# Performance work log

Measured on AMD Instinct MI355X. Metric: run time of the kernel, lower is better.

The kernel has to match this reference:

```python
import jax, jax.numpy as jnp
import numpy as np

NUM_LEVELS = 16
RESOLUTIONS = np.array([16, 18, 20, 22, 25, 27, 30, 34, 38, 42, 47, 52, 58, 64, 72, 80], dtype=np.int32)
OFFSETS = np.concatenate([np.zeros(1, np.int64), np.cumsum(RESOLUTIONS.astype(np.int64) ** 3)]).astype(np.int32)
BATCH = 2
C_IN = 16
C_OUT = 16
K = 3


def setup_inputs() -> dict:
    key = jax.random.key(0)
    k1, k2, k3 = jax.random.split(key, 3)
    n_total = int(OFFSETS[-1])  # 1846083 embeddings across all levels
    inp = jax.random.normal(k1, (BATCH, n_total, C_IN), dtype=jnp.float32)
    weight = 0.1 * jax.random.normal(k2, (NUM_LEVELS, K, K, K, C_IN, C_OUT), dtype=jnp.float32)
    bias = 0.01 * jax.random.uniform(k3, (NUM_LEVELS, C_OUT), dtype=jnp.float32)
    # offsets / resolutions are static int buffers (kept as numpy so they stay
    # concrete under jit, mirroring registered int buffers in the torch module)
    return {"input": inp, "weight": weight, "bias": bias,
            "offsets": OFFSETS, "resolutions": RESOLUTIONS}


def _conv_all_levels(inp, weight, bias, offsets, resolutions):
    # inp: [B, N_total, C_in]; per level l the slice offsets[l]:offsets[l+1]
    # is a dense R_l^3 grid flattened x-fastest (idx = x + y*R + z*R^2).
    B = inp.shape[0]
    dn = ('NDHWC', 'DHWIO', 'NDHWC')
    outs = []
    for l in range(NUM_LEVELS):
        R = int(resolutions[l])
        off = int(offsets[l])
        x = inp[:, off:off + R ** 3, :].reshape(B, R, R, R, C_IN)  # [B,Z,Y,X,Cin]
        y = jax.lax.conv_general_dilated(
            x, weight[l], window_strides=(1, 1, 1), padding='SAME',
            dimension_numbers=dn)  # zero-padded 3x3x3 neighborhood gather
        y = y + bias[l]
        outs.append(y.reshape(B, R ** 3, C_OUT))
    return jnp.concatenate(outs, axis=1)  # [B, N_total, C_out]


def reference(input, weight, bias, offsets, resolutions):
    return _conv_all_levels(input, weight, bias, offsets, resolutions)
```

## Files before the change

### kernel.cpp

```cpp
#include <hip/hip_runtime.h>

#define NLVL 16
#define NTOT 1846083
#define NBLK 4376

typedef float  f32x4  __attribute__((ext_vector_type(4)));
typedef __bf16 bf16x8 __attribute__((ext_vector_type(8)));
typedef __bf16 bf16x4 __attribute__((ext_vector_type(4)));
typedef unsigned int u32x4 __attribute__((ext_vector_type(4)));

__constant__ int c_R[NLVL]   = {16,18,20,22,25,27,30,34,38,42,47,52,58,64,72,80};
__constant__ int c_off[NLVL] = {0,4096,9928,17928,28576,44201,63884,90884,130188,185060,259148,362971,503579,698691,960835,1334083};
__constant__ int c_czy[NLVL] = {4,5,5,6,7,7,8,9,10,11,12,13,15,16,18,20};
__constant__ int c_cx[NLVL]  = {1,2,2,2,2,2,2,3,3,3,3,4,4,4,5,5};
__constant__ int c_base[17]  = {0,1000,1900,2412,2892,3308,3524,3722,3902,4064,4128,4184,4240,4288,4328,4368,4376};

__device__ __align__(16) unsigned short g_bfrag[NLVL*3*5*64*8];

__global__ void prep_bfrag(const float* __restrict__ wgt) {
    int tid = blockIdx.x * 256 + threadIdx.x;
    if (tid >= NLVL*3*5*64) return;
    int lane = tid & 63;
    int p    = (tid >> 6) % 5;
    int d    = (tid / (5*64)) % 3;
    int l    = tid / (3*5*64);
    int quad = lane >> 4, co = lane & 15;
    unsigned short v[8];
#pragma unroll
    for (int j = 0; j < 8; ++j) {
        int k   = quad*8 + j;
        int tip = k >> 4;
        int ci  = k & 15;
        int t2  = 2*p + tip;
        float f = (t2 < 9) ? wgt[((l*27 + d*9 + t2)*16 + ci)*16 + co] : 0.f;
        v[j] = __builtin_bit_cast(unsigned short, (__bf16)f);
    }
    u32x4 pk;
    pk[0] = (unsigned)v[0] | ((unsigned)v[1] << 16);
    pk[1] = (unsigned)v[2] | ((unsigned)v[3] << 16);
    pk[2] = (unsigned)v[4] | ((unsigned)v[5] << 16);
    pk[3] = (unsigned)v[6] | ((unsigned)v[7] << 16);
    *(u32x4*)&g_bfrag[(size_t)tid*8] = pk;
}

__global__ __launch_bounds__(256, 3)
void conv_kernel(const float* __restrict__ in,
                 const float* __restrict__ bias,
                 float* __restrict__ out) {
    __shared__ __align__(16) __bf16 slab[2*1728];

    const int bid = blockIdx.x;
    int idx = 0;
#pragma unroll
    for (int i = 1; i < 16; ++i) if (bid >= c_base[i]) idx = i;
    const int l = 15 - idx;
    const int R = c_R[l], off = c_off[l], czy = c_czy[l], cx = c_cx[l];

    int local = bid - c_base[idx];
    int per_b = czy*cx*cx;
    int bb = local / per_b;         int r1 = local - bb*per_b;
    int zt = r1 / (czy*cx);         int r2 = r1 - zt*(czy*cx);
    int yt = r2 / cx;               int xt = r2 - yt*cx;
    const int z0 = zt*16;
    const int z1 = (z0 + 16 < R) ? z0 + 16 : R;
    const int y0 = yt*4, x0 = xt*16;

    const int t    = threadIdx.x;
    const int lane = t & 63;
    const int wv   = t >> 6;
    const int quad = lane >> 4;
    const int co   = lane & 15;
    const int m    = lane & 15;
    const int qh   = quad >> 1;

    bf16x8 bfr[15];
#pragma unroll
    for (int d = 0; d < 3; ++d)
#pragma unroll
        for (int p = 0; p < 5; ++p)
            bfr[d*5+p] = *(const bf16x8*)&g_bfrag[(size_t)(((l*3 + d)*5 + p)*64 + lane)*8];

    const int albase = wv*576 + m*32 + (quad & 1)*16;
    int aoff[5];
    {
        const int T0[5] = {0, 64, 608, 1152, 1216};
        const int T1[5] = {32, 576, 640, 1184, 1216};
#pragma unroll
        for (int p = 0; p < 5; ++p) aoff[p] = albase + (qh ? T1[p] : T0[p]);
    }

    const long zs = (long)R*R*16;
    long g0 = 0, g1 = 0; int lo0 = 0, lo1 = 0; bool yx0 = false, yx1 = false;
    {
        int c = t;
        int yp = c/72; int rem = c - yp*72; int xp = rem>>2; int ci4 = (rem&3)<<2;
        lo0 = (yp*18 + xp)*16 + ci4;
        int y = y0 + yp - 1, x = x0 + xp - 1;
        yx0 = ((unsigned)y < (unsigned)R) && ((unsigned)x < (unsigned)R);
        g0 = ((long)bb*NTOT + off)*16 + ((long)y*R + x)*16 + ci4;
    }
    const bool has1 = (t < 176);
    if (has1) {
        int c = t + 256;
        int yp = c/72; int rem = c - yp*72; int xp = rem>>2; int ci4 = (rem&3)<<2;
        lo1 = (yp*18 + xp)*16 + ci4;
        int y = y0 + yp - 1, x = x0 + xp - 1;
        yx1 = ((unsigned)y < (unsigned)R) && ((unsigned)x < (unsigned)R);
        g1 = ((long)bb*NTOT + off)*16 + ((long)y*R + x)*16 + ci4;
    }

    __bf16* sbr = slab;
    __bf16* sbw = slab + 1728;

    {
        int zn = z0 - 1;
        bool zok = (unsigned)zn < (unsigned)R;
        f32x4 v0 = {0,0,0,0}, v1 = {0,0,0,0};
        if (zok && yx0) v0 = *(const f32x4*)(in + g0 + (long)zn*zs);
        if (has1 && zok && yx1) v1 = *(const f32x4*)(in + g1 + (long)zn*zs);
        bf16x4 h0 = {(__bf16)v0[0],(__bf16)v0[1],(__bf16)v0[2],(__bf16)v0[3]};
        *(bf16x4*)(sbr + lo0) = h0;
        if (has1) {
            bf16x4 h1 = {(__bf16)v1[0],(__bf16)v1[1],(__bf16)v1[2],(__bf16)v1[3]};
            *(bf16x4*)(sbr + lo1) = h1;
        }
    }
    __syncthreads();

    const bool ywok = (y0 + wv) < R;
    const float bv = bias[(l << 4) + co];
    const long obase = ((long)bb*NTOT + off)*16;

    f32x4 accA = {0,0,0,0}, accB = {0,0,0,0}, accC = {0,0,0,0};
    const int steps = z1 - z0 + 2;

    for (int i = 0; i < steps; ++i) {
        const int zp = z0 - 1 + i;
        const int zn = zp + 1;
        const bool sok = (zn <= z1);

        f32x4 v0 = {0,0,0,0}, v1 = {0,0,0,0};
        if (sok) {
            bool zok = (unsigned)zn < (unsigned)R;
            if (zok && yx0) v0 = *(const f32x4*)(in + g0 + (long)zn*zs);
            if (has1 && zok && yx1) v1 = *(const f32x4*)(in + g1 + (long)zn*zs);
        }

        const char* sb = (const char*)sbr;
#pragma unroll
        for (int p = 0; p < 5; ++p) {
            bf16x8 a = *(const bf16x8*)(sb + aoff[p]);
            accC = __builtin_amdgcn_mfma_f32_16x16x32_bf16(a, bfr[p],      accC, 0, 0, 0);
            accB = __builtin_amdgcn_mfma_f32_16x16x32_bf16(a, bfr[5+p],  accB, 0, 0, 0);
            accA = __builtin_amdgcn_mfma_f32_16x16x32_bf16(a, bfr[10+p], accA, 0, 0, 0);
        }

        if (sok) {
            bf16x4 h0 = {(__bf16)v0[0],(__bf16)v0[1],(__bf16)v0[2],(__bf16)v0[3]};
            *(bf16x4*)(sbw + lo0) = h0;
            if (has1) {
                bf16x4 h1 = {(__bf16)v1[0],(__bf16)v1[1],(__bf16)v1[2],(__bf16)v1[3]};
                *(bf16x4*)(sbw + lo1) = h1;
            }
        }

        if (i >= 2 && ywok) {
            int z = zp - 1;
            long rb = obase + (((long)z*R + (y0 + wv))*R)*16 + co;
#pragma unroll
            for (int rr = 0; rr < 4; ++rr) {
                int x = x0 + quad*4 + rr;
                if (x < R) out[rb + (long)x*16] = accA[rr] + bv;
            }
        }

        accA = accB; accB = accC;
        accC = (f32x4){0,0,0,0};

        __syncthreads();
        __bf16* tmp = sbr; sbr = sbw; sbw = tmp;
    }
}

extern "C" void kernel_launch(void* const* d_in, const int* in_sizes, int n_in,
                              void* d_out, int out_size, void* d_ws, size_t ws_size,
                              hipStream_t stream) {
    const float* inp = (const float*)d_in[0];
    const float* wgt = (const float*)d_in[1];
    const float* bia = (const float*)d_in[2];
    float* out = (float*)d_out;
    prep_bfrag<<<dim3((NLVL*3*5*64 + 255)/256), dim3(256), 0, stream>>>(wgt);
    conv_kernel<<<dim3(NBLK), dim3(256), 0, stream>>>(inp, bia, out);
}
```

Measured before the change: 439.6 us.

## Prefetch input slices two planes ahead and vectorize output stores via swapped MFMA

Restructures the z-plane loop so global loads for plane z+2 are issued while plane z+1 is converted and written to shared memory, using two register sets rotated by a 2-way unrolled loop. This hides global load latency behind the MFMA work. It also swaps the MFMA operand order so each lane holds four consecutive output channels, which allows one 16-byte store per lane with a vector bias add instead of four scalar strided stores. The full __syncthreads is replaced with an LDS-only waitcnt plus a raw barrier, so in-flight global loads are not drained at each step. The cost is extra registers.

```diff
diff --git a/kernel.cpp b/kernel.cpp
--- a/kernel.cpp
+++ b/kernel.cpp
@@ -69,7 +69,6 @@
     const int lane = t & 63;
     const int wv   = t >> 6;
     const int quad = lane >> 4;
-    const int co   = lane & 15;
     const int m    = lane & 15;
     const int qh   = quad >> 1;
 
@@ -112,74 +111,81 @@
     __bf16* sbr = slab;
     __bf16* sbw = slab + 1728;
 
+    const f32x4 zero4 = {0,0,0,0};
+    f32x4 rA0 = zero4, rA1 = zero4, rB0 = zero4, rB1 = zero4;
+
     {
         int zn = z0 - 1;
-        bool zok = (unsigned)zn < (unsigned)R;
-        f32x4 v0 = {0,0,0,0}, v1 = {0,0,0,0};
-        if (zok && yx0) v0 = *(const f32x4*)(in + g0 + (long)zn*zs);
-        if (has1 && zok && yx1) v1 = *(const f32x4*)(in + g1 + (long)zn*zs);
-        bf16x4 h0 = {(__bf16)v0[0],(__bf16)v0[1],(__bf16)v0[2],(__bf16)v0[3]};
+        if (zn >= 0) {
+            if (yx0) rA0 = *(const f32x4*)(in + g0 + (long)zn*zs);
+            if (has1 && yx1) rA1 = *(const f32x4*)(in + g1 + (long)zn*zs);
+        }
+        if (yx0) rB0 = *(const f32x4*)(in + g0 + (long)z0*zs);
+        if (has1 && yx1) rB1 = *(const f32x4*)(in + g1 + (long)z0*zs);
+        bf16x4 h0 = {(__bf16)rA0[0],(__bf16)rA0[1],(__bf16)rA0[2],(__bf16)rA0[3]};
         *(bf16x4*)(sbr + lo0) = h0;
         if (has1) {
-            bf16x4 h1 = {(__bf16)v1[0],(__bf16)v1[1],(__bf16)v1[2],(__bf16)v1[3]};
+            bf16x4 h1 = {(__bf16)rA1[0],(__bf16)rA1[1],(__bf16)rA1[2],(__bf16)rA1[3]};
             *(bf16x4*)(sbr + lo1) = h1;
         }
     }
-    __syncthreads();
+    asm volatile("s_waitcnt lgkmcnt(0)" ::: "memory");
+    __builtin_amdgcn_s_barrier();
+    asm volatile("" ::: "memory");
 
     const bool ywok = (y0 + wv) < R;
-    const float bv = bias[(l << 4) + co];
+    const f32x4 bv4 = *(const f32x4*)(bias + (l << 4) + (quad << 2));
     const long obase = ((long)bb*NTOT + off)*16;
-
-    f32x4 accA = {0,0,0,0}, accB = {0,0,0,0}, accC = {0,0,0,0};
     const int steps = z1 - z0 + 2;
 
-    for (int i = 0; i < steps; ++i) {
-        const int zp = z0 - 1 + i;
-        const int zn = zp + 1;
-        const bool sok = (zn <= z1);
-
-        f32x4 v0 = {0,0,0,0}, v1 = {0,0,0,0};
-        if (sok) {
-            bool zok = (unsigned)zn < (unsigned)R;
-            if (zok && yx0) v0 = *(const f32x4*)(in + g0 + (long)zn*zs);
-            if (has1 && zok && yx1) v1 = *(const f32x4*)(in + g1 + (long)zn*zs);
-        }
-
+    f32x4 accA = zero4, accB = zero4, accC = zero4;
+
+    auto stepf = [&](int i, f32x4& w0, f32x4& w1, f32x4& l0, f32x4& l1) {
+        const int zl = z0 + 1 + i;
+        if (zl <= z1) {
+            const bool zok = zl < R;
+            l0 = zero4; l1 = zero4;
+            if (zok && yx0) l0 = *(const f32x4*)(in + g0 + (long)zl*zs);
+            if (has1 && zok && yx1) l1 = *(const f32x4*)(in + g1 + (long)zl*zs);
+        }
+        if (i <= steps - 2) {
+            bf16x4 h0 = {(__bf16)w0[0],(__bf16)w0[1],(__bf16)w0[2],(__bf16)w0[3]};
+            *(bf16x4*)(sbw + lo0) = h0;
+            if (has1) {
+                bf16x4 h1 = {(__bf16)w1[0],(__bf16)w1[1],(__bf16)w1[2],(__bf16)w1[3]};
+                *(bf16x4*)(sbw + lo1) = h1;
+            }
+        }
         const char* sb = (const char*)sbr;
 #pragma unroll
         for (int p = 0; p < 5; ++p) {
             bf16x8 a = *(const bf16x8*)(sb + aoff[p]);
-            accC = __builtin_amdgcn_mfma_f32_16x16x32_bf16(a, bfr[p],      accC, 0, 0, 0);
-            accB = __builtin_amdgcn_mfma_f32_16x16x32_bf16(a, bfr[5+p],  accB, 0, 0, 0);
-            accA = __builtin_amdgcn_mfma_f32_16x16x32_bf16(a, bfr[10+p], accA, 0, 0, 0);
-        }
-
-        if (sok) {
-            bf16x4 h0 = {(__bf16)v0[0],(__bf16)v0[1],(__bf16)v0[2],(__bf16)v0[3]};
-            *(bf16x4*)(sbw + lo0) = h0;
-            if (has1) {
-                bf16x4 h1 = {(__bf16)v1[0],(__bf16)v1[1],(__bf16)v1[2],(__bf16)v1[3]};
-                *(bf16x4*)(sbw + lo1) = h1;
+            accC = __builtin_amdgcn_mfma_f32_16x16x32_bf16(bfr[p],    a, accC, 0, 0, 0);
+            accB = __builtin_amdgcn_mfma_f32_16x16x32_bf16(bfr[5+p],  a, accB, 0, 0, 0);
+            accA = __builtin_amdgcn_mfma_f32_16x16x32_bf16(bfr[10+p], a, accA, 0, 0, 0);
+        }
+        if (i >= 2 && ywok) {
+            const int x = x0 + m;
+            if (x < R) {
+                const int z = z0 - 2 + i;
+                long rb = obase + (((long)z*R + (y0 + wv))*(long)R + x)*16 + (quad << 2);
+                f32x4 o = accA + bv4;
+                *(f32x4*)(out + rb) = o;
             }
         }
-
-        if (i >= 2 && ywok) {
-            int z = zp - 1;
-            long rb = obase + (((long)z*R + (y0 + wv))*R)*16 + co;
-#pragma unroll
-            for (int rr = 0; rr < 4; ++rr) {
-                int x = x0 + quad*4 + rr;
-                if (x < R) out[rb + (long)x*16] = accA[rr] + bv;
-            }
-        }
-
-        accA = accB; accB = accC;
-        accC = (f32x4){0,0,0,0};
-
-        __syncthreads();
-        __bf16* tmp = sbr; sbr = sbw; sbw = tmp;
-    }
+        accA = accB; accB = accC; accC = zero4;
+        asm volatile("s_waitcnt lgkmcnt(0)" ::: "memory");
+        __builtin_amdgcn_s_barrier();
+        asm volatile("" ::: "memory");
+        __bf16* t_ = sbr; sbr = sbw; sbw = t_;
+    };
+
+    int i = 0;
+    for (; i + 1 < steps; i += 2) {
+        stepf(i,     rB0, rB1, rA0, rA1);
+        stepf(i + 1, rA0, rA1, rB0, rB1);
+    }
+    if (i < steps) stepf(i, rB0, rB1, rA0, rA1);
 }
 
 extern "C" void kernel_launch(void* const* d_in, const int* in_sizes, int n_in,
```

After: 429.4 us. 2.3% less time.

## Stream fp32 input slabs into LDS via async global_load_lds with triple buffering

Applied to the files above, without the earlier changes.

Replaces the register-staged load plus bf16 conversion into a double-buffered bf16 slab with direct async global-to-LDS loads into a triple-buffered fp32 slab, converting to bf16 when reading A fragments. Tiles grow to 8 y-rows per block (two rows per wave), halving the block count and reusing the weight fragments across two MFMA chains. MFMA operands are swapped so the output is stored as 16-byte vectors, and the barrier waits on vmcnt to keep one slab in flight. This costs more LDS per block (fp32 instead of bf16, three buffers) and adds conversion work on every LDS read, while raising launch bounds to 4 waves per SIMD.

```diff
diff --git a/kernel.cpp b/kernel.cpp
--- a/kernel.cpp
+++ b/kernel.cpp
@@ -2,20 +2,21 @@
 
 #define NLVL 16
 #define NTOT 1846083
-#define NBLK 4376
+#define NBLK 2254
 
 typedef float  f32x4  __attribute__((ext_vector_type(4)));
 typedef __bf16 bf16x8 __attribute__((ext_vector_type(8)));
-typedef __bf16 bf16x4 __attribute__((ext_vector_type(4)));
+typedef unsigned int u32;
 typedef unsigned int u32x4 __attribute__((ext_vector_type(4)));
 
 __constant__ int c_R[NLVL]   = {16,18,20,22,25,27,30,34,38,42,47,52,58,64,72,80};
 __constant__ int c_off[NLVL] = {0,4096,9928,17928,28576,44201,63884,90884,130188,185060,259148,362971,503579,698691,960835,1334083};
-__constant__ int c_czy[NLVL] = {4,5,5,6,7,7,8,9,10,11,12,13,15,16,18,20};
+__constant__ int c_czy[NLVL] = {2,3,3,3,4,4,4,5,5,6,6,7,8,8,9,10};
 __constant__ int c_cx[NLVL]  = {1,2,2,2,2,2,2,3,3,3,3,4,4,4,5,5};
-__constant__ int c_base[17]  = {0,1000,1900,2412,2892,3308,3524,3722,3902,4064,4128,4184,4240,4288,4328,4368,4376};
+__constant__ int c_base[17]  = {0,500,950,1206,1462,1686,1794,1902,1992,2082,2114,2146,2178,2202,2226,2250,2254};
 
 __device__ __align__(16) unsigned short g_bfrag[NLVL*3*5*64*8];
+__device__ __align__(16) float g_zero[4] = {0.f, 0.f, 0.f, 0.f};
 
 __global__ void prep_bfrag(const float* __restrict__ wgt) {
     int tid = blockIdx.x * 256 + threadIdx.x;
@@ -36,18 +37,24 @@
         v[j] = __builtin_bit_cast(unsigned short, (__bf16)f);
     }
     u32x4 pk;
-    pk[0] = (unsigned)v[0] | ((unsigned)v[1] << 16);
-    pk[1] = (unsigned)v[2] | ((unsigned)v[3] << 16);
-    pk[2] = (unsigned)v[4] | ((unsigned)v[5] << 16);
-    pk[3] = (unsigned)v[6] | ((unsigned)v[7] << 16);
+    pk[0] = (u32)v[0] | ((u32)v[1] << 16);
+    pk[1] = (u32)v[2] | ((u32)v[3] << 16);
+    pk[2] = (u32)v[4] | ((u32)v[5] << 16);
+    pk[3] = (u32)v[6] | ((u32)v[7] << 16);
     *(u32x4*)&g_bfrag[(size_t)tid*8] = pk;
 }
 
-__global__ __launch_bounds__(256, 3)
+__device__ __forceinline__ void gll16(const void* g, void* l) {
+    __builtin_amdgcn_global_load_lds(
+        (const __attribute__((address_space(1))) u32*)g,
+        (__attribute__((address_space(3))) u32*)l, 16, 0, 0);
+}
+
+__global__ __launch_bounds__(256, 4)
 void conv_kernel(const float* __restrict__ in,
                  const float* __restrict__ bias,
                  float* __restrict__ out) {
-    __shared__ __align__(16) __bf16 slab[2*1728];
+    __shared__ __align__(16) float slab[3*2880];
 
     const int bid = blockIdx.x;
     int idx = 0;
@@ -63,13 +70,12 @@
     int yt = r2 / cx;               int xt = r2 - yt*cx;
     const int z0 = zt*16;
     const int z1 = (z0 + 16 < R) ? z0 + 16 : R;
-    const int y0 = yt*4, x0 = xt*16;
+    const int y0 = yt*8, x0 = xt*16;
 
     const int t    = threadIdx.x;
     const int lane = t & 63;
     const int wv   = t >> 6;
     const int quad = lane >> 4;
-    const int co   = lane & 15;
     const int m    = lane & 15;
     const int qh   = quad >> 1;
 
@@ -80,106 +86,116 @@
         for (int p = 0; p < 5; ++p)
             bfr[d*5+p] = *(const bf16x8*)&g_bfrag[(size_t)(((l*3 + d)*5 + p)*64 + lane)*8];
 
-    const int albase = wv*576 + m*32 + (quad & 1)*16;
+    const int albase = wv*2304 + m*64 + (quad & 1)*32;
     int aoff[5];
     {
-        const int T0[5] = {0, 64, 608, 1152, 1216};
-        const int T1[5] = {32, 576, 640, 1184, 1216};
+        const int T0[5] = {0, 128, 1216, 2304, 2432};
+        const int T1[5] = {64, 1152, 1280, 2368, 2432};
 #pragma unroll
         for (int p = 0; p < 5; ++p) aoff[p] = albase + (qh ? T1[p] : T0[p]);
     }
 
     const long zs = (long)R*R*16;
-    long g0 = 0, g1 = 0; int lo0 = 0, lo1 = 0; bool yx0 = false, yx1 = false;
+    const long gstart = ((long)bb*NTOT + off)*16;
+    const float* cur[3]; bool ok[3];
     {
-        int c = t;
-        int yp = c/72; int rem = c - yp*72; int xp = rem>>2; int ci4 = (rem&3)<<2;
-        lo0 = (yp*18 + xp)*16 + ci4;
-        int y = y0 + yp - 1, x = x0 + xp - 1;
-        yx0 = ((unsigned)y < (unsigned)R) && ((unsigned)x < (unsigned)R);
-        g0 = ((long)bb*NTOT + off)*16 + ((long)y*R + x)*16 + ci4;
-    }
-    const bool has1 = (t < 176);
-    if (has1) {
-        int c = t + 256;
-        int yp = c/72; int rem = c - yp*72; int xp = rem>>2; int ci4 = (rem&3)<<2;
-        lo1 = (yp*18 + xp)*16 + ci4;
-        int y = y0 + yp - 1, x = x0 + xp - 1;
-        yx1 = ((unsigned)y < (unsigned)R) && ((unsigned)x < (unsigned)R);
-        g1 = ((long)bb*NTOT + off)*16 + ((long)y*R + x)*16 + ci4;
-    }
-
-    __bf16* sbr = slab;
-    __bf16* sbw = slab + 1728;
+#pragma unroll
+        for (int s = 0; s < 3; ++s) {
+            int c = t + s*256;
+            int yp = c/72; int rem = c - yp*72; int xp = rem>>2; int ci4 = (rem&3)<<2;
+            int y = y0 + yp - 1, x = x0 + xp - 1;
+            ok[s] = ((unsigned)y < (unsigned)R) && ((unsigned)x < (unsigned)R);
+            cur[s] = in + gstart + ((long)y*R + x)*16 + ci4 + (long)(z0-1)*zs;
+        }
+    }
+    const bool has2 = (t < 208);
+
+    float* b0 = slab;
+    float* b1 = slab + 2880;
+    float* b2 = slab + 5760;
+
+    const float* zv = g_zero;
+    char* const lw = (char*)0 + wv*1024;
+    const int wvo = wv*1024;
 
     {
-        int zn = z0 - 1;
-        bool zok = (unsigned)zn < (unsigned)R;
-        f32x4 v0 = {0,0,0,0}, v1 = {0,0,0,0};
-        if (zok && yx0) v0 = *(const f32x4*)(in + g0 + (long)zn*zs);
-        if (has1 && zok && yx1) v1 = *(const f32x4*)(in + g1 + (long)zn*zs);
-        bf16x4 h0 = {(__bf16)v0[0],(__bf16)v0[1],(__bf16)v0[2],(__bf16)v0[3]};
-        *(bf16x4*)(sbr + lo0) = h0;
-        if (has1) {
-            bf16x4 h1 = {(__bf16)v1[0],(__bf16)v1[1],(__bf16)v1[2],(__bf16)v1[3]};
-            *(bf16x4*)(sbr + lo1) = h1;
-        }
-    }
-    __syncthreads();
-
-    const bool ywok = (y0 + wv) < R;
-    const float bv = bias[(l << 4) + co];
-    const long obase = ((long)bb*NTOT + off)*16;
-
-    f32x4 accA = {0,0,0,0}, accB = {0,0,0,0}, accC = {0,0,0,0};
+        bool zrA = (z0 - 1) >= 0;
+        gll16(zrA && ok[0] ? cur[0] : zv, (char*)b0 + wvo);
+        gll16(zrA && ok[1] ? cur[1] : zv, (char*)b0 + wvo + 4096);
+        if (has2) gll16(zrA && ok[2] ? cur[2] : zv, (char*)b0 + wvo + 8192);
+        gll16(ok[0] ? cur[0] + zs : zv, (char*)b1 + wvo);
+        gll16(ok[1] ? cur[1] + zs : zv, (char*)b1 + wvo + 4096);
+        if (has2) gll16(ok[2] ? cur[2] + zs : zv, (char*)b1 + wvo + 8192);
+        cur[0] += 2*zs; cur[1] += 2*zs; cur[2] += 2*zs;
+    }
+    asm volatile("s_waitcnt vmcnt(3)" ::: "memory");
+    __builtin_amdgcn_s_barrier();
+    asm volatile("" ::: "memory");
+
+    const int yo0 = y0 + 2*wv, yo1 = yo0 + 1;
+    const bool yw0 = yo0 < R, yw1 = yo1 < R;
+    const bool xok = (x0 + m) < R;
+    const f32x4 bv4 = *(const f32x4*)(bias + (l << 4) + (quad << 2));
+
+    float* so0 = out + gstart + (((long)z0*R + yo0)*(long)R + x0 + m)*16 + (quad << 2);
+    float* so1 = so0 + (long)R*16;
+
+    const f32x4 zero4 = {0,0,0,0};
+    f32x4 aA0 = zero4, aB0 = zero4, aC0 = zero4;
+    f32x4 aA1 = zero4, aB1 = zero4, aC1 = zero4;
+    f32x4 aO0 = zero4, aO1 = zero4;
+
     const int steps = z1 - z0 + 2;
 
+#pragma unroll 1
     for (int i = 0; i < steps; ++i) {
-        const int zp = z0 - 1 + i;
-        const int zn = zp + 1;
-        const bool sok = (zn <= z1);
-
-        f32x4 v0 = {0,0,0,0}, v1 = {0,0,0,0};
-        if (sok) {
-            bool zok = (unsigned)zn < (unsigned)R;
-            if (zok && yx0) v0 = *(const f32x4*)(in + g0 + (long)zn*zs);
-            if (has1 && zok && yx1) v1 = *(const f32x4*)(in + g1 + (long)zn*zs);
-        }
-
-        const char* sb = (const char*)sbr;
+        if (i >= 3) {
+            if (yw0) { f32x4 o = aO0 + bv4; if (xok) *(f32x4*)so0 = o; }
+            if (yw1) { f32x4 o = aO1 + bv4; if (xok) *(f32x4*)so1 = o; }
+            so0 += zs; so1 += zs;
+        }
+
+        {
+            const int zn = z0 + 1 + i;
+            const bool zr = (zn <= z1) && (zn < R);
+            gll16(zr && ok[0] ? cur[0] : zv, (char*)b2 + wvo);
+            gll16(zr && ok[1] ? cur[1] : zv, (char*)b2 + wvo + 4096);
+            if (has2) gll16(zr && ok[2] ? cur[2] : zv, (char*)b2 + wvo + 8192);
+            cur[0] += zs; cur[1] += zs; cur[2] += zs;
+        }
+
+        const char* sb = (const char*)b0;
 #pragma unroll
         for (int p = 0; p < 5; ++p) {
-            bf16x8 a = *(const bf16x8*)(sb + aoff[p]);
-            accC = __builtin_amdgcn_mfma_f32_16x16x32_bf16(a, bfr[p],      accC, 0, 0, 0);
-            accB = __builtin_amdgcn_mfma_f32_16x16x32_bf16(a, bfr[5+p],  accB, 0, 0, 0);
-            accA = __builtin_amdgcn_mfma_f32_16x16x32_bf16(a, bfr[10+p], accA, 0, 0, 0);
-        }
-
-        if (sok) {
-            bf16x4 h0 = {(__bf16)v0[0],(__bf16)v0[1],(__bf16)v0[2],(__bf16)v0[3]};
-            *(bf16x4*)(sbw + lo0) = h0;
-            if (has1) {
-                bf16x4 h1 = {(__bf16)v1[0],(__bf16)v1[1],(__bf16)v1[2],(__bf16)v1[3]};
-                *(bf16x4*)(sbw + lo1) = h1;
-            }
-        }
-
-        if (i >= 2 && ywok) {
-            int z = zp - 1;
-            long rb = obase + (((long)z*R + (y0 + wv))*R)*16 + co;
-#pragma unroll
-            for (int rr = 0; rr < 4; ++rr) {
-                int x = x0 + quad*4 + rr;
-                if (x < R) out[rb + (long)x*16] = accA[rr] + bv;
-            }
-        }
-
-        accA = accB; accB = accC;
-        accC = (f32x4){0,0,0,0};
-
-        __syncthreads();
-        __bf16* tmp = sbr; sbr = sbw; sbw = tmp;
-    }
+            const char* sa = sb + aoff[p];
+            f32x4 q00 = *(const f32x4*)(sa);
+            f32x4 q01 = *(const f32x4*)(sa + 16);
+            f32x4 q10 = *(const f32x4*)(sa + 1152);
+            f32x4 q11 = *(const f32x4*)(sa + 1168);
+            bf16x8 A0 = {(__bf16)q00[0],(__bf16)q00[1],(__bf16)q00[2],(__bf16)q00[3],
+                         (__bf16)q01[0],(__bf16)q01[1],(__bf16)q01[2],(__bf16)q01[3]};
+            bf16x8 A1 = {(__bf16)q10[0],(__bf16)q10[1],(__bf16)q10[2],(__bf16)q10[3],
+                         (__bf16)q11[0],(__bf16)q11[1],(__bf16)q11[2],(__bf16)q11[3]};
+            aC0 = __builtin_amdgcn_mfma_f32_16x16x32_bf16(bfr[p],    A0, aC0, 0, 0, 0);
+            aC1 = __builtin_amdgcn_mfma_f32_16x16x32_bf16(bfr[p],    A1, aC1, 0, 0, 0);
+            aB0 = __builtin_amdgcn_mfma_f32_16x16x32_bf16(bfr[5+p],  A0, aB0, 0, 0, 0);
+            aB1 = __builtin_amdgcn_mfma_f32_16x16x32_bf16(bfr[5+p],  A1, aB1, 0, 0, 0);
+            aA0 = __builtin_amdgcn_mfma_f32_16x16x32_bf16(bfr[10+p], A0, aA0, 0, 0, 0);
+            aA1 = __builtin_amdgcn_mfma_f32_16x16x32_bf16(bfr[10+p], A1, aA1, 0, 0, 0);
+        }
+
+        aO0 = aA0; aA0 = aB0; aB0 = aC0; aC0 = zero4;
+        aO1 = aA1; aA1 = aB1; aB1 = aC1; aC1 = zero4;
+
+        asm volatile("s_waitcnt vmcnt(3)" ::: "memory");
+        __builtin_amdgcn_s_barrier();
+        asm volatile("" ::: "memory");
+
+        float* tmp = b0; b0 = b1; b1 = b2; b2 = tmp;
+    }
+
+    if (yw0) { f32x4 o = aO0 + bv4; if (xok) *(f32x4*)so0 = o; }
+    if (yw1) { f32x4 o = aO1 + bv4; if (xok) *(f32x4*)so1 = o; }
 }
 
 extern "C" void kernel_launch(void* const* d_in, const int* in_sizes, int n_in,
```

Result: no change. 439.5 us (-0.0%).

## Give each wave its own tile with private LDS slab and register prefetch

Applied to the files above, without the earlier changes.

Each wavefront now processes a full 16x4x16 tile independently with its own double-buffered LDS slab, which removes the block-wide __syncthreads per z-step. Global loads are issued one z-plane ahead into register arrays, and the loop is unrolled by six with rotating accumulators. The MFMA operand order is swapped so outputs come out as 16-byte vector stores with a vector bias add. This raises register pressure (launch bounds drop to 2 blocks/SM) and cuts the grid to 1094 blocks, which can unbalance load because tiles of different levels share a block. No wave-level sync separates the LDS write from the next read, so it relies on in-wave ordering, and 32-bit byte offsets into the input are assumed sufficient.

```diff
diff --git a/kernel.cpp b/kernel.cpp
--- a/kernel.cpp
+++ b/kernel.cpp
@@ -2,11 +2,13 @@
 
 #define NLVL 16
 #define NTOT 1846083
-#define NBLK 4376
+#define NTILE 4376
+#define NBLOCK 1094
 
 typedef float  f32x4  __attribute__((ext_vector_type(4)));
 typedef __bf16 bf16x8 __attribute__((ext_vector_type(8)));
 typedef __bf16 bf16x4 __attribute__((ext_vector_type(4)));
+typedef unsigned int u32;
 typedef unsigned int u32x4 __attribute__((ext_vector_type(4)));
 
 __constant__ int c_R[NLVL]   = {16,18,20,22,25,27,30,34,38,42,47,52,58,64,72,80};
@@ -36,27 +38,31 @@
         v[j] = __builtin_bit_cast(unsigned short, (__bf16)f);
     }
     u32x4 pk;
-    pk[0] = (unsigned)v[0] | ((unsigned)v[1] << 16);
-    pk[1] = (unsigned)v[2] | ((unsigned)v[3] << 16);
-    pk[2] = (unsigned)v[4] | ((unsigned)v[5] << 16);
-    pk[3] = (unsigned)v[6] | ((unsigned)v[7] << 16);
+    pk[0] = (u32)v[0] | ((u32)v[1] << 16);
+    pk[1] = (u32)v[2] | ((u32)v[3] << 16);
+    pk[2] = (u32)v[4] | ((u32)v[5] << 16);
+    pk[3] = (u32)v[6] | ((u32)v[7] << 16);
     *(u32x4*)&g_bfrag[(size_t)tid*8] = pk;
 }
 
-__global__ __launch_bounds__(256, 3)
+__global__ __launch_bounds__(256, 2)
 void conv_kernel(const float* __restrict__ in,
                  const float* __restrict__ bias,
                  float* __restrict__ out) {
-    __shared__ __align__(16) __bf16 slab[2*1728];
-
-    const int bid = blockIdx.x;
+    __shared__ __align__(16) char slab[4*8192];
+
+    const int t    = threadIdx.x;
+    const int lane = t & 63;
+    const int wv   = t >> 6;
+
+    const int tid4 = blockIdx.x*4 + wv;
     int idx = 0;
 #pragma unroll
-    for (int i = 1; i < 16; ++i) if (bid >= c_base[i]) idx = i;
+    for (int i = 1; i < 16; ++i) if (tid4 >= c_base[i]) idx = i;
     const int l = 15 - idx;
     const int R = c_R[l], off = c_off[l], czy = c_czy[l], cx = c_cx[l];
 
-    int local = bid - c_base[idx];
+    int local = tid4 - c_base[idx];
     int per_b = czy*cx*cx;
     int bb = local / per_b;         int r1 = local - bb*per_b;
     int zt = r1 / (czy*cx);         int r2 = r1 - zt*(czy*cx);
@@ -64,12 +70,9 @@
     const int z0 = zt*16;
     const int z1 = (z0 + 16 < R) ? z0 + 16 : R;
     const int y0 = yt*4, x0 = xt*16;
-
-    const int t    = threadIdx.x;
-    const int lane = t & 63;
-    const int wv   = t >> 6;
+    const int steps = z1 - z0 + 2;
+
     const int quad = lane >> 4;
-    const int co   = lane & 15;
     const int m    = lane & 15;
     const int qh   = quad >> 1;
 
@@ -80,106 +83,123 @@
         for (int p = 0; p < 5; ++p)
             bfr[d*5+p] = *(const bf16x8*)&g_bfrag[(size_t)(((l*3 + d)*5 + p)*64 + lane)*8];
 
-    const int albase = wv*576 + m*32 + (quad & 1)*16;
-    int aoff[5];
+    const char* sbase = (const char*)slab + wv*8192;
+    const char* arA[5];
     {
         const int T0[5] = {0, 64, 608, 1152, 1216};
         const int T1[5] = {32, 576, 640, 1184, 1216};
-#pragma unroll
-        for (int p = 0; p < 5; ++p) aoff[p] = albase + (qh ? T1[p] : T0[p]);
-    }
-
-    const long zs = (long)R*R*16;
-    long g0 = 0, g1 = 0; int lo0 = 0, lo1 = 0; bool yx0 = false, yx1 = false;
+        const int ab = m*32 + (quad & 1)*16;
+#pragma unroll
+        for (int p = 0; p < 5; ++p) arA[p] = sbase + ab + (qh ? T1[p] : T0[p]);
+    }
+    char* wbase = (char*)slab + wv*8192 + lane*8;
+
+    const int  zsE = R*R*16;
+    const u32  zsB = (u32)zsE*4;
+    const long gstartE = ((long)bb*NTOT + off)*16;
+
+    u32 cur[7]; bool okk[7];
+#pragma unroll
+    for (int s = 0; s < 7; ++s) {
+        int c = lane + s*64;
+        int yp = c/72; int rem = c - yp*72; int xp = rem>>2; int ci4 = (rem&3)<<2;
+        int y = y0 + yp - 1, x = x0 + xp - 1;
+        okk[s] = (c < 432) && ((unsigned)y < (unsigned)R) && ((unsigned)x < (unsigned)R);
+        long e = gstartE + (long)(z0-1)*zsE + ((long)y*R + x)*16 + ci4;
+        cur[s] = (u32)(e*4);
+    }
+
+    const f32x4 z4 = {0,0,0,0};
+    f32x4 LA[7], LB[7];
+
     {
-        int c = t;
-        int yp = c/72; int rem = c - yp*72; int xp = rem>>2; int ci4 = (rem&3)<<2;
-        lo0 = (yp*18 + xp)*16 + ci4;
-        int y = y0 + yp - 1, x = x0 + xp - 1;
-        yx0 = ((unsigned)y < (unsigned)R) && ((unsigned)x < (unsigned)R);
-        g0 = ((long)bb*NTOT + off)*16 + ((long)y*R + x)*16 + ci4;
-    }
-    const bool has1 = (t < 176);
-    if (has1) {
-        int c = t + 256;
-        int yp = c/72; int rem = c - yp*72; int xp = rem>>2; int ci4 = (rem&3)<<2;
-        lo1 = (yp*18 + xp)*16 + ci4;
-        int y = y0 + yp - 1, x = x0 + xp - 1;
-        yx1 = ((unsigned)y < (unsigned)R) && ((unsigned)x < (unsigned)R);
-        g1 = ((long)bb*NTOT + off)*16 + ((long)y*R + x)*16 + ci4;
-    }
-
-    __bf16* sbr = slab;
-    __bf16* sbw = slab + 1728;
-
-    {
-        int zn = z0 - 1;
-        bool zok = (unsigned)zn < (unsigned)R;
-        f32x4 v0 = {0,0,0,0}, v1 = {0,0,0,0};
-        if (zok && yx0) v0 = *(const f32x4*)(in + g0 + (long)zn*zs);
-        if (has1 && zok && yx1) v1 = *(const f32x4*)(in + g1 + (long)zn*zs);
-        bf16x4 h0 = {(__bf16)v0[0],(__bf16)v0[1],(__bf16)v0[2],(__bf16)v0[3]};
-        *(bf16x4*)(sbr + lo0) = h0;
-        if (has1) {
-            bf16x4 h1 = {(__bf16)v1[0],(__bf16)v1[1],(__bf16)v1[2],(__bf16)v1[3]};
-            *(bf16x4*)(sbr + lo1) = h1;
+        const bool zrA = (z0 > 0);
+#pragma unroll
+        for (int s = 0; s < 7; ++s) { f32x4 v = z4; if (zrA && okk[s]) v = *(const f32x4*)((const char*)in + cur[s]); LA[s] = v; }
+#pragma unroll
+        for (int s = 0; s < 7; ++s) cur[s] += zsB;
+#pragma unroll
+        for (int s = 0; s < 7; ++s) { f32x4 v = z4; if (okk[s]) v = *(const f32x4*)((const char*)in + cur[s]); LB[s] = v; }
+#pragma unroll
+        for (int s = 0; s < 7; ++s) cur[s] += zsB;
+#pragma unroll
+        for (int s = 0; s < 7; ++s) {
+            bf16x4 h = {(__bf16)LA[s][0],(__bf16)LA[s][1],(__bf16)LA[s][2],(__bf16)LA[s][3]};
+            *(bf16x4*)(wbase + s*512) = h;
         }
     }
-    __syncthreads();
-
-    const bool ywok = (y0 + wv) < R;
-    const float bv = bias[(l << 4) + co];
-    const long obase = ((long)bb*NTOT + off)*16;
-
-    f32x4 accA = {0,0,0,0}, accB = {0,0,0,0}, accC = {0,0,0,0};
-    const int steps = z1 - z0 + 2;
-
-    for (int i = 0; i < steps; ++i) {
-        const int zp = z0 - 1 + i;
-        const int zn = zp + 1;
-        const bool sok = (zn <= z1);
-
-        f32x4 v0 = {0,0,0,0}, v1 = {0,0,0,0};
-        if (sok) {
-            bool zok = (unsigned)zn < (unsigned)R;
-            if (zok && yx0) v0 = *(const f32x4*)(in + g0 + (long)zn*zs);
-            if (has1 && zok && yx1) v1 = *(const f32x4*)(in + g1 + (long)zn*zs);
-        }
-
-        const char* sb = (const char*)sbr;
-#pragma unroll
-        for (int p = 0; p < 5; ++p) {
-            bf16x8 a = *(const bf16x8*)(sb + aoff[p]);
-            accC = __builtin_amdgcn_mfma_f32_16x16x32_bf16(a, bfr[p],      accC, 0, 0, 0);
-            accB = __builtin_amdgcn_mfma_f32_16x16x32_bf16(a, bfr[5+p],  accB, 0, 0, 0);
-            accA = __builtin_amdgcn_mfma_f32_16x16x32_bf16(a, bfr[10+p], accA, 0, 0, 0);
-        }
-
-        if (sok) {
-            bf16x4 h0 = {(__bf16)v0[0],(__bf16)v0[1],(__bf16)v0[2],(__bf16)v0[3]};
-            *(bf16x4*)(sbw + lo0) = h0;
-            if (has1) {
-                bf16x4 h1 = {(__bf16)v1[0],(__bf16)v1[1],(__bf16)v1[2],(__bf16)v1[3]};
-                *(bf16x4*)(sbw + lo1) = h1;
-            }
-        }
-
-        if (i >= 2 && ywok) {
-            int z = zp - 1;
-            long rb = obase + (((long)z*R + (y0 + wv))*R)*16 + co;
-#pragma unroll
-            for (int rr = 0; rr < 4; ++rr) {
-                int x = x0 + quad*4 + rr;
-                if (x < R) out[rb + (long)x*16] = accA[rr] + bv;
-            }
-        }
-
-        accA = accB; accB = accC;
-        accC = (f32x4){0,0,0,0};
-
-        __syncthreads();
-        __bf16* tmp = sbr; sbr = sbw; sbw = tmp;
-    }
+
+    const bool xok = (x0 + m) < R;
+    bool ywr[4];
+#pragma unroll
+    for (int r = 0; r < 4; ++r) ywr[r] = (y0 + r) < R;
+    const f32x4 bv4 = *(const f32x4*)(bias + (l << 4) + (quad << 2));
+
+    float* so[4];
+#pragma unroll
+    for (int r = 0; r < 4; ++r)
+        so[r] = out + gstartE + (((long)z0*R + (y0 + r))*(long)R + (x0 + m))*16 + (quad << 2);
+
+    f32x4 acc0[4], acc1[4], acc2[4];
+#pragma unroll
+    for (int r = 0; r < 4; ++r) { acc0[r] = z4; acc1[r] = z4; acc2[r] = z4; }
+
+    int zl = z0 + 1;
+
+#define BODY(II, PAR, LN, LO, AX, AY, AZ, ENST)                                         \
+    {                                                                                   \
+        const bool zr = (zl <= z1) && (zl < R);                                         \
+        _Pragma("unroll")                                                               \
+        for (int s = 0; s < 7; ++s) {                                                   \
+            f32x4 v = z4;                                                               \
+            if (zr && okk[s]) v = *(const f32x4*)((const char*)in + cur[s]);            \
+            LN[s] = v;                                                                  \
+        }                                                                               \
+        { u32 a_ = zr ? zsB : 0u;                                                       \
+          _Pragma("unroll") for (int s = 0; s < 7; ++s) cur[s] += a_; }                 \
+        ++zl;                                                                           \
+        _Pragma("unroll")                                                               \
+        for (int p = 0; p < 5; ++p) {                                                   \
+            _Pragma("unroll")                                                           \
+            for (int r = 0; r < 4; ++r) {                                               \
+                bf16x8 af = *(const bf16x8*)(arA[p] + (PAR)*4096 + r*576);              \
+                AX[r] = __builtin_amdgcn_mfma_f32_16x16x32_bf16(bfr[p],    af, AX[r], 0,0,0); \
+                AY[r] = __builtin_amdgcn_mfma_f32_16x16x32_bf16(bfr[5+p],  af, AY[r], 0,0,0); \
+                AZ[r] = __builtin_amdgcn_mfma_f32_16x16x32_bf16(bfr[10+p], af, AZ[r], 0,0,0); \
+            }                                                                           \
+        }                                                                               \
+        _Pragma("unroll")                                                               \
+        for (int s = 0; s < 7; ++s) {                                                   \
+            bf16x4 h = {(__bf16)LO[s][0],(__bf16)LO[s][1],(__bf16)LO[s][2],(__bf16)LO[s][3]}; \
+            *(bf16x4*)(wbase + ((PAR)^1)*4096 + s*512) = h;                             \
+        }                                                                               \
+        if ((ENST) && (II) < steps) {                                                   \
+            _Pragma("unroll")                                                           \
+            for (int r = 0; r < 4; ++r) {                                               \
+                if (ywr[r] && xok) { f32x4 o_ = AZ[r] + bv4; *(f32x4*)so[r] = o_; }     \
+                so[r] += zsE;                                                           \
+            }                                                                           \
+        }                                                                               \
+        _Pragma("unroll")                                                               \
+        for (int r = 0; r < 4; ++r) AZ[r] = z4;                                         \
+    }
+
+    BODY(0, 0, LA, LB, acc0, acc2, acc1, 0)
+    BODY(1, 1, LB, LA, acc1, acc0, acc2, 0)
+    BODY(2, 0, LA, LB, acc2, acc1, acc0, 1)
+    BODY(3, 1, LB, LA, acc0, acc2, acc1, 1)
+    BODY(4, 0, LA, LB, acc1, acc0, acc2, 1)
+    BODY(5, 1, LB, LA, acc2, acc1, acc0, 1)
+#pragma unroll 1
+    for (int i = 6; i < steps; i += 6) {
+        BODY(i+0, 0, LA, LB, acc0, acc2, acc1, 1)
+        BODY(i+1, 1, LB, LA, acc1, acc0, acc2, 1)
+        BODY(i+2, 0, LA, LB, acc2, acc1, acc0, 1)
+        BODY(i+3, 1, LB, LA, acc0, acc2, acc1, 1)
+        BODY(i+4, 0, LA, LB, acc1, acc0, acc2, 1)
+        BODY(i+5, 1, LB, LA, acc2, acc1, acc0, 1)
+    }
+#undef BODY
 }
 
 extern "C" void kernel_launch(void* const* d_in, const int* in_sizes, int n_in,
@@ -190,5 +210,5 @@
     const float* bia = (const float*)d_in[2];
     float* out = (float*)d_out;
     prep_bfrag<<<dim3((NLVL*3*5*64 + 255)/256), dim3(256), 0, stream>>>(wgt);
-    conv_kernel<<<dim3(NBLK), dim3(256), 0, stream>>>(inp, bia, out);
+    conv_kernel<<<dim3(NBLOCK), dim3(256), 0, stream>>>(inp, bia, out);
 }
```

Result: faster. 426.1 us (-3.1%).
